# Performance work log

Hardware: AMD Instinct MI355X
Metric: run time of the kernel (lower is better)

Reference implementation:

```python
import jax, jax.numpy as jnp
import numpy as np

N_NODES = 50000
N_EDGES = 800000
IN_FEATS = 256
HIDDEN = 256
NUM_CLASSES = 64


def setup_inputs() -> dict:
    key = jax.random.key(0)
    k1, k2, k3, k4 = jax.random.split(key, 4)
    features = jax.random.normal(k1, (N_NODES, IN_FEATS), dtype=jnp.float32)
    edge_index = jax.random.randint(k2, (2, N_EDGES), 0, N_NODES, dtype=jnp.int32)
    W1 = jax.random.normal(k3, (IN_FEATS, HIDDEN), dtype=jnp.float32) * (1.0 / np.sqrt(IN_FEATS))
    b1 = jnp.zeros((HIDDEN,), dtype=jnp.float32)
    W2 = jax.random.normal(k4, (HIDDEN, NUM_CLASSES), dtype=jnp.float32) * (1.0 / np.sqrt(HIDDEN))
    b2 = jnp.zeros((NUM_CLASSES,), dtype=jnp.float32)
    return {"features": features, "edge_index": edge_index, "W1": W1, "b1": b1, "W2": W2, "b2": b2}


def reference(features, edge_index, W1, b1, W2, b2):
    # Two-layer GCN: h = A_hat @ relu(A_hat @ X W1 + b1) W2 + b2
    # A_hat uses symmetric degree normalization 1/sqrt(d_src * d_dst)
    N = features.shape[0]
    src, dst = edge_index[0], edge_index[1]
    ones = jnp.ones((src.shape[0],), dtype=features.dtype)
    deg_out = jax.ops.segment_sum(ones, src, num_segments=N)  # out-degree per node
    deg_in = jax.ops.segment_sum(ones, dst, num_segments=N)   # in-degree per node
    inv_sqrt_out = jax.lax.rsqrt(jnp.maximum(deg_out, 1.0))
    inv_sqrt_in = jax.lax.rsqrt(jnp.maximum(deg_in, 1.0))
    edge_norm = (inv_sqrt_out[src] * inv_sqrt_in[dst])[:, None]  # [E,1]

    def gcn_layer(x, W, b):
        h = x @ W                      # transform first (reduces message width)
        msg = h[src] * edge_norm       # [E, out]
        agg = jax.ops.segment_sum(msg, dst, num_segments=N)
        return agg + b

    h = jax.nn.relu(gcn_layer(features, W1, b1))
    return gcn_layer(h, W2, b2)
```

## Files before the change

kernel.cpp:

```cpp
#include <hip/hip_runtime.h>

#define NN 50000
#define MPAD 50048
#define NE 800000
#define SCAN_BLOCKS 49

typedef short short8 __attribute__((ext_vector_type(8)));
typedef float f32x4 __attribute__((ext_vector_type(4)));

__device__ __forceinline__ unsigned short f2bf(float x) {
    unsigned u = __builtin_bit_cast(unsigned, x);
    u += 0x7FFFu + ((u >> 16) & 1u);
    return (unsigned short)(u >> 16);
}
__device__ __forceinline__ float bf2f(unsigned short h) {
    unsigned u = ((unsigned)h) << 16;
    return __builtin_bit_cast(float, u);
}
__device__ __forceinline__ void gld16(const void* g, void* l) {
    __builtin_amdgcn_global_load_lds(
        (const __attribute__((address_space(1))) unsigned int*)g,
        (__attribute__((address_space(3))) unsigned int*)l, 16, 0, 0);
}
__device__ __forceinline__ void nt_store8(void* p, ushort4 v) {
    __builtin_nontemporal_store(__builtin_bit_cast(unsigned long long, v),
                                (unsigned long long*)p);
}


__global__ __launch_bounds__(256) void count_kernel(const int* __restrict__ src,
    const int* __restrict__ dst, int* __restrict__ cnt_out, int* __restrict__ cnt_in, int E)
{
    int e = blockIdx.x * 256 + threadIdx.x;
    if (e < E) {
        atomicAdd(&cnt_out[src[e]], 1);
        atomicAdd(&cnt_in[dst[e]], 1);
    }
}

__global__ __launch_bounds__(256) void inv_kernel(const int* __restrict__ cnt_out,
    const int* __restrict__ cnt_in, float* __restrict__ inv_out, float* __restrict__ inv_in, int n)
{
    int i = blockIdx.x * 256 + threadIdx.x;
    if (i < n) {
        inv_out[i] = rsqrtf(fmaxf((float)cnt_out[i], 1.0f));
        inv_in[i]  = rsqrtf(fmaxf((float)cnt_in[i], 1.0f));
    }
}

__global__ __launch_bounds__(256) void scanA_kernel(const int* __restrict__ cnt,
    int* __restrict__ bsum)
{
    __shared__ int sm[256];
    int b = blockIdx.x, tid = threadIdx.x;
    int base = b * 1024 + tid * 4;
    int s = 0;
    #pragma unroll
    for (int i = 0; i < 4; ++i) {
        int idx = base + i;
        if (idx < NN) s += cnt[idx];
    }
    sm[tid] = s;
    __syncthreads();
    for (int off = 128; off > 0; off >>= 1) {
        if (tid < off) sm[tid] += sm[tid + off];
        __syncthreads();
    }
    if (tid == 0) bsum[b] = sm[0];
}

__global__ __launch_bounds__(64) void scanB_kernel(const int* __restrict__ bsum,
    int* __restrict__ bexcl)
{
    int tid = threadIdx.x;
    int orig = (tid < SCAN_BLOCKS) ? bsum[tid] : 0;
    int v = orig;
    #pragma unroll
    for (int off = 1; off < 64; off <<= 1) {
        int u = __shfl_up(v, off, 64);
        if (tid >= off) v += u;
    }
    if (tid < SCAN_BLOCKS) bexcl[tid] = v - orig;
}

__global__ __launch_bounds__(256) void scanC_kernel(const int* __restrict__ cnt,
    const int* __restrict__ bexcl, int* __restrict__ rs)
{
    __shared__ int wsum[4];
    int b = blockIdx.x, tid = threadIdx.x;
    int lane = tid & 63, wv = tid >> 6;
    int base = b * 1024 + tid * 4;
    int v[4]; int s = 0;
    #pragma unroll
    for (int i = 0; i < 4; ++i) {
        int idx = base + i;
        v[i] = (idx < NN) ? cnt[idx] : 0;
        s += v[i];
    }
    int inc = s;
    #pragma unroll
    for (int off = 1; off < 64; off <<= 1) {
        int u = __shfl_up(inc, off, 64);
        if (lane >= off) inc += u;
    }
    if (lane == 63) wsum[wv] = inc;
    __syncthreads();
    int wo = 0;
    for (int i = 0; i < wv; ++i) wo += wsum[i];
    int run = wo + (inc - s) + bexcl[b];
    #pragma unroll
    for (int i = 0; i < 4; ++i) {
        int idx = base + i;
        if (idx < NN) { rs[idx] = run; run += v[i]; }
    }
}

__global__ __launch_bounds__(256) void fill_kernel(const int* __restrict__ src,
    const int* __restrict__ dst, int* __restrict__ rs, int* __restrict__ csr_src, int E)
{
    int e = blockIdx.x * 256 + threadIdx.x;
    if (e < E) {
        int slot = atomicAdd(&rs[dst[e]], 1);
        csr_src[slot] = src[e];
    }
}

__global__ __launch_bounds__(256) void splitX_kernel(const float* __restrict__ X,
    unsigned short* __restrict__ Xh, unsigned short* __restrict__ Xl)
{
    int i = blockIdx.x * 256 + threadIdx.x;
    if (i >= NN * 32) return;
    int r = i >> 5, c = i & 31;
    const float* src = X + (size_t)r * 256 + c * 8;
    float4 a0 = *(const float4*)src;
    float4 a1 = *(const float4*)(src + 4);
    float xs[8] = {a0.x, a0.y, a0.z, a0.w, a1.x, a1.y, a1.z, a1.w};
    short8 hv, lv;
    #pragma unroll
    for (int t = 0; t < 8; ++t) {
        unsigned short h = f2bf(xs[t]);
        hv[t] = (short)h;
        lv[t] = (short)f2bf(xs[t] - bf2f(h));
    }
    size_t off = (size_t)r * 256 + (c >> 3) * 64 + (((c & 7) ^ (r & 7)) * 8);
    *(short8*)&Xh[off] = hv;
    *(short8*)&Xl[off] = lv;
}

__global__ __launch_bounds__(256) void splitW_kernel(const float* __restrict__ W,
    unsigned short* __restrict__ BT, int N)
{
    int i = blockIdx.x * 256 + threadIdx.x;
    if (i >= N * 32) return;
    int col = i >> 5, kc = i & 31;
    short8 hv, lv;
    #pragma unroll
    for (int j = 0; j < 8; ++j) {
        float x = W[(size_t)(kc * 8 + j) * N + col];
        unsigned short h = f2bf(x);
        hv[j] = (short)h;
        lv[j] = (short)f2bf(x - bf2f(h));
    }
    size_t base = (size_t)col * 512;
    size_t o = (kc >> 3) * 64 + (((kc & 7) ^ (col & 7)) * 8);
    *(short8*)&BT[base + o] = hv;
    *(short8*)&BT[base + 256 + o] = lv;
}

template<int BN>
__global__ __launch_bounds__(256) void gemm_sp_kernel(
    const unsigned short* __restrict__ Ah, const unsigned short* __restrict__ Al,
    const unsigned short* __restrict__ BT, const float* __restrict__ inv_out,
    unsigned short* __restrict__ C, int M, int Ntot)
{
    constexpr int WN = BN / 2;
    constexpr int NF = WN / 16;
    constexpr int BI = BN / 32;
    __shared__ unsigned short Ash[128 * 64];
    __shared__ unsigned short Asl[128 * 64];
    __shared__ unsigned short Bsh[BN * 64];
    __shared__ unsigned short Bsl[BN * 64];
    const int tid = threadIdx.x;
    const int w = tid >> 6, lane = tid & 63;
    const int wm = w >> 1, wn = w & 1;
    const int r = lane & 15, kg = lane >> 4;
    const int rowbase = blockIdx.x * 128;
    const int colbase = blockIdx.y * BN;

    f32x4 acc[4][NF] = {};

    for (int kb = 0; kb < 4; ++kb) {
        #pragma unroll
        for (int i = 0; i < 4; ++i) {
            int ct = (w * 4 + i) * 64 + lane;
            int row = ct >> 3, c = ct & 7;
            size_t goff = (size_t)(rowbase + row) * 256 + kb * 64 + c * 8;
            gld16(Ah + goff, (unsigned short*)Ash + (size_t)ct * 8);
            gld16(Al + goff, (unsigned short*)Asl + (size_t)ct * 8);
        }
        #pragma unroll
        for (int i = 0; i < BI; ++i) {
            int ct = (w * BI + i) * 64 + lane;
            int col = ct >> 3, c = ct & 7;
            size_t goff = (size_t)(colbase + col) * 512 + kb * 64 + c * 8;
            gld16(BT + goff, (unsigned short*)Bsh + (size_t)ct * 8);
            gld16(BT + goff + 256, (unsigned short*)Bsl + (size_t)ct * 8);
        }
        __syncthreads();
        #pragma unroll
        for (int ks = 0; ks < 2; ++ks) {
            short8 ahf[4], alf[4];
            #pragma unroll
            for (int mf = 0; mf < 4; ++mf) {
                int row = wm * 64 + mf * 16 + r;
                int lo = row * 64 + (((ks * 4 + kg) ^ (row & 7)) * 8);
                ahf[mf] = *(const short8*)&Ash[lo];
                alf[mf] = *(const short8*)&Asl[lo];
            }
            #pragma unroll
            for (int nf = 0; nf < NF; ++nf) {
                int col = wn * WN + nf * 16 + r;
                int lo = col * 64 + (((ks * 4 + kg) ^ (col & 7)) * 8);
                short8 bh = *(const short8*)&Bsh[lo];
                short8 bl = *(const short8*)&Bsl[lo];
                #pragma unroll
                for (int mf = 0; mf < 4; ++mf) {
                    acc[mf][nf] = __builtin_amdgcn_mfma_f32_16x16x32_bf16(ahf[mf], bh, acc[mf][nf], 0, 0, 0);
                    acc[mf][nf] = __builtin_amdgcn_mfma_f32_16x16x32_bf16(alf[mf], bh, acc[mf][nf], 0, 0, 0);
                    acc[mf][nf] = __builtin_amdgcn_mfma_f32_16x16x32_bf16(ahf[mf], bl, acc[mf][nf], 0, 0, 0);
                }
            }
        }
        __syncthreads();
    }

    #pragma unroll
    for (int mf = 0; mf < 4; ++mf) {
        #pragma unroll
        for (int reg = 0; reg < 4; ++reg) {
            int orow = rowbase + wm * 64 + mf * 16 + kg * 4 + reg;
            if (orow >= M) continue;
            float sc = inv_out[orow];
            #pragma unroll
            for (int nf = 0; nf < NF; ++nf) {
                int ocol = colbase + wn * WN + nf * 16 + r;
                C[(size_t)orow * Ntot + ocol] = f2bf(acc[mf][nf][reg] * sc);
            }
        }
    }
}

__global__ __launch_bounds__(256) void gather256_kernel(const unsigned short* __restrict__ t1,
    const int* __restrict__ csr_src, const int* __restrict__ rs,
    const float* __restrict__ inv_in, const float* __restrict__ b1,
    unsigned short* __restrict__ Ah2, unsigned short* __restrict__ Al2)
{
    int n = (int)((blockIdx.x * 256 + threadIdx.x) >> 6);
    int lane = threadIdx.x & 63;
    if (n >= NN) return;
    int begin = (n == 0) ? 0 : rs[n - 1];
    int end = rs[n];
    float a0 = 0.f, a1 = 0.f, a2 = 0.f, a3 = 0.f;
    int j = begin;
    for (; j + 8 <= end; j += 8) {
        int s0 = csr_src[j],     s1 = csr_src[j + 1], s2 = csr_src[j + 2], s3 = csr_src[j + 3];
        int s4 = csr_src[j + 4], s5 = csr_src[j + 5], s6 = csr_src[j + 6], s7 = csr_src[j + 7];
        ushort4 v0 = *(const ushort4*)&t1[(size_t)s0 * 256 + lane * 4];
        ushort4 v1 = *(const ushort4*)&t1[(size_t)s1 * 256 + lane * 4];
        ushort4 v2 = *(const ushort4*)&t1[(size_t)s2 * 256 + lane * 4];
        ushort4 v3 = *(const ushort4*)&t1[(size_t)s3 * 256 + lane * 4];
        ushort4 v4 = *(const ushort4*)&t1[(size_t)s4 * 256 + lane * 4];
        ushort4 v5 = *(const ushort4*)&t1[(size_t)s5 * 256 + lane * 4];
        ushort4 v6 = *(const ushort4*)&t1[(size_t)s6 * 256 + lane * 4];
        ushort4 v7 = *(const ushort4*)&t1[(size_t)s7 * 256 + lane * 4];
        a0 += bf2f(v0.x); a1 += bf2f(v0.y); a2 += bf2f(v0.z); a3 += bf2f(v0.w);
        a0 += bf2f(v1.x); a1 += bf2f(v1.y); a2 += bf2f(v1.z); a3 += bf2f(v1.w);
        a0 += bf2f(v2.x); a1 += bf2f(v2.y); a2 += bf2f(v2.z); a3 += bf2f(v2.w);
        a0 += bf2f(v3.x); a1 += bf2f(v3.y); a2 += bf2f(v3.z); a3 += bf2f(v3.w);
        a0 += bf2f(v4.x); a1 += bf2f(v4.y); a2 += bf2f(v4.z); a3 += bf2f(v4.w);
        a0 += bf2f(v5.x); a1 += bf2f(v5.y); a2 += bf2f(v5.z); a3 += bf2f(v5.w);
        a0 += bf2f(v6.x); a1 += bf2f(v6.y); a2 += bf2f(v6.z); a3 += bf2f(v6.w);
        a0 += bf2f(v7.x); a1 += bf2f(v7.y); a2 += bf2f(v7.z); a3 += bf2f(v7.w);
    }
    for (; j < end; ++j) {
        int s = csr_src[j];
        ushort4 v = *(const ushort4*)&t1[(size_t)s * 256 + lane * 4];
        a0 += bf2f(v.x); a1 += bf2f(v.y); a2 += bf2f(v.z); a3 += bf2f(v.w);
    }
    float win = inv_in[n];
    int f0 = lane * 4;
    float4 bb = *(const float4*)&b1[f0];
    float x0 = fmaxf(fmaf(a0, win, bb.x), 0.f);
    float x1 = fmaxf(fmaf(a1, win, bb.y), 0.f);
    float x2 = fmaxf(fmaf(a2, win, bb.z), 0.f);
    float x3 = fmaxf(fmaf(a3, win, bb.w), 0.f);
    unsigned short h0 = f2bf(x0), h1 = f2bf(x1), h2 = f2bf(x2), h3 = f2bf(x3);
    ushort4 hv = {h0, h1, h2, h3};
    ushort4 lv = {f2bf(x0 - bf2f(h0)), f2bf(x1 - bf2f(h1)),
                  f2bf(x2 - bf2f(h2)), f2bf(x3 - bf2f(h3))};
    int kb = f0 >> 6, c = (f0 >> 3) & 7, e = f0 & 7;
    size_t off = (size_t)n * 256 + kb * 64 + ((c ^ (n & 7)) * 8) + e;
    nt_store8(&Ah2[off], hv);
    nt_store8(&Al2[off], lv);
}

__global__ __launch_bounds__(256) void gather64_kernel(const unsigned short* __restrict__ t2,
    const int* __restrict__ csr_src, const int* __restrict__ rs,
    const float* __restrict__ inv_in, const float* __restrict__ b2,
    float* __restrict__ out)
{
    int n = (int)((blockIdx.x * 256 + threadIdx.x) >> 6);
    int lane = threadIdx.x & 63;
    if (n >= NN) return;
    int begin = (n == 0) ? 0 : rs[n - 1];
    int end = rs[n];
    float acc = 0.f;
    int j = begin;
    for (; j + 8 <= end; j += 8) {
        int s0 = csr_src[j],     s1 = csr_src[j + 1], s2 = csr_src[j + 2], s3 = csr_src[j + 3];
        int s4 = csr_src[j + 4], s5 = csr_src[j + 5], s6 = csr_src[j + 6], s7 = csr_src[j + 7];
        float v0 = bf2f(t2[(size_t)s0 * 64 + lane]);
        float v1 = bf2f(t2[(size_t)s1 * 64 + lane]);
        float v2 = bf2f(t2[(size_t)s2 * 64 + lane]);
        float v3 = bf2f(t2[(size_t)s3 * 64 + lane]);
        float v4 = bf2f(t2[(size_t)s4 * 64 + lane]);
        float v5 = bf2f(t2[(size_t)s5 * 64 + lane]);
        float v6 = bf2f(t2[(size_t)s6 * 64 + lane]);
        float v7 = bf2f(t2[(size_t)s7 * 64 + lane]);
        acc += v0; acc += v1; acc += v2; acc += v3;
        acc += v4; acc += v5; acc += v6; acc += v7;
    }
    for (; j < end; ++j) {
        int s = csr_src[j];
        acc += bf2f(t2[(size_t)s * 64 + lane]);
    }
    float o = fmaf(acc, inv_in[n], b2[lane]);
    __builtin_nontemporal_store(o, &out[(size_t)n * 64 + lane]);
}

extern "C" void kernel_launch(void* const* d_in, const int* in_sizes, int n_in,
                              void* d_out, int out_size, void* d_ws, size_t ws_size,
                              hipStream_t stream)
{
    const float* features = (const float*)d_in[0];
    const int*   edge_index = (const int*)d_in[1];
    const float* W1 = (const float*)d_in[2];
    const float* b1 = (const float*)d_in[3];
    const float* W2 = (const float*)d_in[4];
    const float* b2 = (const float*)d_in[5];
    float* out = (float*)d_out;
    const int* src = edge_index;
    const int* dst = edge_index + NE;

    char* p = (char*)d_ws;
    int* cnt_out = (int*)p;            p += (size_t)NN * 4;
    int* cnt_in  = (int*)p;            p += (size_t)NN * 4;
    float* inv_out = (float*)p;        p += (size_t)NN * 4;
    float* inv_in  = (float*)p;        p += (size_t)NN * 4;
    int* rs      = (int*)p;            p += (size_t)NN * 4;
    int* csr_src = (int*)p;            p += (size_t)NE * 4;
    int* bsum    = (int*)p;            p += 64 * 4;
    int* bexcl   = (int*)p;            p += 64 * 4;
    unsigned short* W1T = (unsigned short*)p;  p += (size_t)256 * 512 * 2;
    unsigned short* W2T = (unsigned short*)p;  p += (size_t)64 * 512 * 2;
    unsigned short* Xh  = (unsigned short*)p;  p += (size_t)MPAD * 256 * 2;
    unsigned short* Xl  = (unsigned short*)p;  p += (size_t)MPAD * 256 * 2;
    unsigned short* t1  = (unsigned short*)p;  p += (size_t)NN * 256 * 2;
    unsigned short* Ah2 = (unsigned short*)p;  p += (size_t)MPAD * 256 * 2;
    unsigned short* Al2 = (unsigned short*)p;  p += (size_t)MPAD * 256 * 2;
    unsigned short* t2  = (unsigned short*)p;  p += (size_t)NN * 64 * 2;

    hipMemsetAsync(cnt_out, 0, 2 * (size_t)NN * sizeof(int), stream);

    count_kernel<<<(NE + 255) / 256, 256, 0, stream>>>(src, dst, cnt_out, cnt_in, NE);
    inv_kernel<<<(NN + 255) / 256, 256, 0, stream>>>(cnt_out, cnt_in, inv_out, inv_in, NN);
    scanA_kernel<<<SCAN_BLOCKS, 256, 0, stream>>>(cnt_in, bsum);
    scanB_kernel<<<1, 64, 0, stream>>>(bsum, bexcl);
    scanC_kernel<<<SCAN_BLOCKS, 256, 0, stream>>>(cnt_in, bexcl, rs);
    fill_kernel<<<(NE + 255) / 256, 256, 0, stream>>>(src, dst, rs, csr_src, NE);

    splitX_kernel<<<(NN * 32 + 255) / 256, 256, 0, stream>>>(features, Xh, Xl);
    splitW_kernel<<<(256 * 32 + 255) / 256, 256, 0, stream>>>(W1, W1T, 256);
    splitW_kernel<<<(64 * 32 + 255) / 256, 256, 0, stream>>>(W2, W2T, 64);

    gemm_sp_kernel<128><<<dim3(MPAD / 128, 2), 256, 0, stream>>>(
        Xh, Xl, W1T, inv_out, t1, NN, 256);

    gather256_kernel<<<(NN * 64 + 255) / 256, 256, 0, stream>>>(
        t1, csr_src, rs, inv_in, b1, Ah2, Al2);

    gemm_sp_kernel<64><<<dim3(MPAD / 128, 1), 256, 0, stream>>>(
        Ah2, Al2, W2T, inv_out, t2, NN, 64);

    gather64_kernel<<<(NN * 64 + 255) / 256, 256, 0, stream>>>(
        t2, csr_src, rs, inv_in, b2, out);
}
```

Measured before the change: 326.9 us.

## Fold inv-degree into scan, merge weight splits, read B fragments from global

Removes the separate inverse-degree kernel by computing rsqrt of in/out degree inside the final scan pass. It also merges the two weight-split launches into one and stores the weights unswizzled in a plain layout. The GEMM no longer stages B tiles in shared memory and instead loads B fragments straight from global memory (small, cache-resident weights). This cuts launches and LDS traffic and raises occupancy, at the risk of higher global and L2 latency inside the MFMA loop.

```diff
diff --git a/kernel.cpp b/kernel.cpp
--- a/kernel.cpp
+++ b/kernel.cpp
@@ -35,16 +35,6 @@
     if (e < E) {
         atomicAdd(&cnt_out[src[e]], 1);
         atomicAdd(&cnt_in[dst[e]], 1);
-    }
-}
-
-__global__ __launch_bounds__(256) void inv_kernel(const int* __restrict__ cnt_out,
-    const int* __restrict__ cnt_in, float* __restrict__ inv_out, float* __restrict__ inv_in, int n)
-{
-    int i = blockIdx.x * 256 + threadIdx.x;
-    if (i < n) {
-        inv_out[i] = rsqrtf(fmaxf((float)cnt_out[i], 1.0f));
-        inv_in[i]  = rsqrtf(fmaxf((float)cnt_in[i], 1.0f));
     }
 }
 
@@ -84,7 +74,8 @@
 }
 
 __global__ __launch_bounds__(256) void scanC_kernel(const int* __restrict__ cnt,
-    const int* __restrict__ bexcl, int* __restrict__ rs)
+    const int* __restrict__ cnt_out, const int* __restrict__ bexcl,
+    int* __restrict__ rs, float* __restrict__ inv_out, float* __restrict__ inv_in)
 {
     __shared__ int wsum[4];
     int b = blockIdx.x, tid = threadIdx.x;
@@ -111,7 +102,11 @@
     #pragma unroll
     for (int i = 0; i < 4; ++i) {
         int idx = base + i;
-        if (idx < NN) { rs[idx] = run; run += v[i]; }
+        if (idx < NN) {
+            rs[idx] = run; run += v[i];
+            inv_in[idx]  = rsqrtf(fmaxf((float)v[i], 1.0f));
+            inv_out[idx] = rsqrtf(fmaxf((float)cnt_out[idx], 1.0f));
+        }
     }
 }
 
@@ -147,24 +142,23 @@
     *(short8*)&Xl[off] = lv;
 }
 
-__global__ __launch_bounds__(256) void splitW_kernel(const float* __restrict__ W,
-    unsigned short* __restrict__ BT, int N)
+__global__ __launch_bounds__(256) void splitW_kernel(const float* __restrict__ W1,
+    const float* __restrict__ W2, unsigned short* __restrict__ W1T,
+    unsigned short* __restrict__ W2T)
 {
     int i = blockIdx.x * 256 + threadIdx.x;
-    if (i >= N * 32) return;
-    int col = i >> 5, kc = i & 31;
-    short8 hv, lv;
+    const float* W; unsigned short* BT; int N; int ii;
+    if (i < 256 * 32) { W = W1; BT = W1T; N = 256; ii = i; }
+    else if (i < 256 * 32 + 64 * 32) { W = W2; BT = W2T; N = 64; ii = i - 256 * 32; }
+    else return;
+    int col = ii >> 5, kc = ii & 31;
     #pragma unroll
     for (int j = 0; j < 8; ++j) {
         float x = W[(size_t)(kc * 8 + j) * N + col];
         unsigned short h = f2bf(x);
-        hv[j] = (short)h;
-        lv[j] = (short)f2bf(x - bf2f(h));
-    }
-    size_t base = (size_t)col * 512;
-    size_t o = (kc >> 3) * 64 + (((kc & 7) ^ (col & 7)) * 8);
-    *(short8*)&BT[base + o] = hv;
-    *(short8*)&BT[base + 256 + o] = lv;
+        BT[(size_t)col * 512 + kc * 8 + j] = h;
+        BT[(size_t)col * 512 + 256 + kc * 8 + j] = f2bf(x - bf2f(h));
+    }
 }
 
 template<int BN>
@@ -175,11 +169,8 @@
 {
     constexpr int WN = BN / 2;
     constexpr int NF = WN / 16;
-    constexpr int BI = BN / 32;
     __shared__ unsigned short Ash[128 * 64];
     __shared__ unsigned short Asl[128 * 64];
-    __shared__ unsigned short Bsh[BN * 64];
-    __shared__ unsigned short Bsl[BN * 64];
     const int tid = threadIdx.x;
     const int w = tid >> 6, lane = tid & 63;
     const int wm = w >> 1, wn = w & 1;
@@ -197,14 +188,6 @@
             size_t goff = (size_t)(rowbase + row) * 256 + kb * 64 + c * 8;
             gld16(Ah + goff, (unsigned short*)Ash + (size_t)ct * 8);
             gld16(Al + goff, (unsigned short*)Asl + (size_t)ct * 8);
-        }
-        #pragma unroll
-        for (int i = 0; i < BI; ++i) {
-            int ct = (w * BI + i) * 64 + lane;
-            int col = ct >> 3, c = ct & 7;
-            size_t goff = (size_t)(colbase + col) * 512 + kb * 64 + c * 8;
-            gld16(BT + goff, (unsigned short*)Bsh + (size_t)ct * 8);
-            gld16(BT + goff + 256, (unsigned short*)Bsl + (size_t)ct * 8);
         }
         __syncthreads();
         #pragma unroll
@@ -219,10 +202,11 @@
             }
             #pragma unroll
             for (int nf = 0; nf < NF; ++nf) {
-                int col = wn * WN + nf * 16 + r;
-                int lo = col * 64 + (((ks * 4 + kg) ^ (col & 7)) * 8);
-                short8 bh = *(const short8*)&Bsh[lo];
-                short8 bl = *(const short8*)&Bsl[lo];
+                const unsigned short* bp = BT
+                    + (size_t)(colbase + wn * WN + nf * 16 + r) * 512
+                    + kb * 64 + ks * 32 + kg * 8;
+                short8 bh = *(const short8*)bp;
+                short8 bl = *(const short8*)(bp + 256);
                 #pragma unroll
                 for (int mf = 0; mf < 4; ++mf) {
                     acc[mf][nf] = __builtin_amdgcn_mfma_f32_16x16x32_bf16(ahf[mf], bh, acc[mf][nf], 0, 0, 0);
@@ -373,15 +357,13 @@
     hipMemsetAsync(cnt_out, 0, 2 * (size_t)NN * sizeof(int), stream);
 
     count_kernel<<<(NE + 255) / 256, 256, 0, stream>>>(src, dst, cnt_out, cnt_in, NE);
-    inv_kernel<<<(NN + 255) / 256, 256, 0, stream>>>(cnt_out, cnt_in, inv_out, inv_in, NN);
     scanA_kernel<<<SCAN_BLOCKS, 256, 0, stream>>>(cnt_in, bsum);
     scanB_kernel<<<1, 64, 0, stream>>>(bsum, bexcl);
-    scanC_kernel<<<SCAN_BLOCKS, 256, 0, stream>>>(cnt_in, bexcl, rs);
+    scanC_kernel<<<SCAN_BLOCKS, 256, 0, stream>>>(cnt_in, cnt_out, bexcl, rs, inv_out, inv_in);
     fill_kernel<<<(NE + 255) / 256, 256, 0, stream>>>(src, dst, rs, csr_src, NE);
 
     splitX_kernel<<<(NN * 32 + 255) / 256, 256, 0, stream>>>(features, Xh, Xl);
-    splitW_kernel<<<(256 * 32 + 255) / 256, 256, 0, stream>>>(W1, W1T, 256);
-    splitW_kernel<<<(64 * 32 + 255) / 256, 256, 0, stream>>>(W2, W2T, 64);
+    splitW_kernel<<<(320 * 32 + 255) / 256, 256, 0, stream>>>(W1, W2, W1T, W2T);
 
     gemm_sp_kernel<128><<<dim3(MPAD / 128, 2), 256, 0, stream>>>(
         Xh, Xl, W1T, inv_out, t1, NN, 256);
```

After: 340.6 us. +4.2%, slower.
